# Kernel tuning notes

Hardware: AMD Instinct MI355X
Metric: run time of the kernel (lower is better)

## Reference

```python
import jax, jax.numpy as jnp
import numpy as np

FEAT = 256          # feat_channels == point_feat_channels == in_channels
STACK = 3           # stacked_convs
NPTS = 9            # num_points -> dcn_kernel = 3
NCLS = 80           # num_classes
GM = 0.1            # gradient_mul
GROUPS = 32         # 32 * 256 // 256
EPS = 1e-5
BIAS_CLS = -float(np.log((1 - 0.01) / 0.01))  # prior_prob focal-bias init


def conv2d(x, w, b=None):
    y = jax.lax.conv_general_dilated(x, w, (1, 1), 'SAME',
                                     dimension_numbers=('NCHW', 'OIHW', 'NCHW'))
    return y if b is None else y + b[None, :, None, None]


def group_norm(x, w, b):
    B, C, H, W = x.shape
    xg = x.reshape(B, GROUPS, C // GROUPS, H, W)
    mu = xg.mean((2, 3, 4), keepdims=True)
    var = xg.var((2, 3, 4), keepdims=True)
    xn = ((xg - mu) * jax.lax.rsqrt(var + EPS)).reshape(B, C, H, W)
    return xn * w[None, :, None, None] + b[None, :, None, None]


def bilinear_sample(x, py, px):
    # x: [B,C,H,W]; py,px: [B,K,H,W] absolute sample coords -> [B,C,K,H,W]
    B, C, H, W = x.shape
    y0 = jnp.floor(py); x0 = jnp.floor(px)
    wy = (py - y0)[:, None]; wx = (px - x0)[:, None]  # [B,1,K,H,W]
    xf = x.reshape(B, C, H * W)

    def gather(yi, xi):
        valid = (yi >= 0) & (yi < H) & (xi >= 0) & (xi < W)
        yic = jnp.clip(yi, 0, H - 1).astype(jnp.int32)
        xic = jnp.clip(xi, 0, W - 1).astype(jnp.int32)
        idx = (yic * W + xic).reshape(B, -1)                       # [B,K*H*W]
        g = jax.vmap(lambda xb, ib: xb[:, ib])(xf, idx)            # [B,C,K*H*W]
        g = g.reshape(B, C, *yi.shape[1:])
        return g * valid[:, None].astype(x.dtype)

    v00 = gather(y0, x0); v01 = gather(y0, x0 + 1)
    v10 = gather(y0 + 1, x0); v11 = gather(y0 + 1, x0 + 1)
    return (v00 * (1 - wy) * (1 - wx) + v01 * (1 - wy) * wx
            + v10 * wy * (1 - wx) + v11 * wy * wx)


def deform_conv(x, offset, w):
    # x: [B,C,H,W]; offset: [B,2K,H,W] as (dy,dx) per kernel point; w: [O,C,kh,kw]
    B, C, H, W = x.shape
    O, _, kh, kw = w.shape
    K = kh * kw
    off = offset.reshape(B, K, 2, H, W)
    by = jnp.repeat(jnp.arange(kh) - (kh - 1) // 2, kw).astype(x.dtype)  # [K]
    bx = jnp.tile(jnp.arange(kw) - (kw - 1) // 2, kh).astype(x.dtype)
    gy = jnp.arange(H, dtype=x.dtype)[None, None, :, None]
    gx = jnp.arange(W, dtype=x.dtype)[None, None, None, :]
    py = gy + by[None, :, None, None] + off[:, :, 0]  # [B,K,H,W]
    px = gx + bx[None, :, None, None] + off[:, :, 1]
    sampled = bilinear_sample(x, py, px)              # [B,C,K,H,W]
    return jnp.einsum('bckhw,ock->bohw', sampled, w.reshape(O, C, K))


def dcn_base_offset():
    base = np.arange(-1, 2, dtype=np.float32)
    y = np.repeat(base, 3); x = np.tile(base, 3)
    return jnp.asarray(np.stack([y, x], axis=1).reshape(1, -1, 1, 1))  # [1,18,1,1]


def setup_inputs() -> dict:
    key = jax.random.key(0)
    ks = jax.random.split(key, 10)
    std = 0.01
    d = {}
    d['features'] = jax.random.normal(ks[0], (4, FEAT, 64, 64), jnp.float32)
    d['cls_w'] = std * jax.random.normal(ks[1], (STACK, FEAT, FEAT, 3, 3), jnp.float32)
    d['reg_w'] = std * jax.random.normal(ks[2], (STACK, FEAT, FEAT, 3, 3), jnp.float32)
    d['cls_gn_w'] = jnp.ones((STACK, FEAT), jnp.float32)
    d['cls_gn_b'] = jnp.zeros((STACK, FEAT), jnp.float32)
    d['reg_gn_w'] = jnp.ones((STACK, FEAT), jnp.float32)
    d['reg_gn_b'] = jnp.zeros((STACK, FEAT), jnp.float32)
    d['init_conv_w'] = std * jax.random.normal(ks[3], (FEAT, FEAT, 3, 3), jnp.float32)
    d['init_conv_b'] = jnp.zeros((FEAT,), jnp.float32)
    d['init_out_w'] = std * jax.random.normal(ks[4], (2 * NPTS, FEAT, 1, 1), jnp.float32)
    d['init_out_b'] = jnp.zeros((2 * NPTS,), jnp.float32)
    d['cls_dcn_w'] = std * jax.random.normal(ks[5], (FEAT, FEAT, 3, 3), jnp.float32)
    d['cls_out_w'] = std * jax.random.normal(ks[6], (NCLS, FEAT, 1, 1), jnp.float32)
    d['cls_out_b'] = jnp.full((NCLS,), BIAS_CLS, jnp.float32)
    d['ref_dcn_w'] = std * jax.random.normal(ks[7], (FEAT, FEAT, 3, 3), jnp.float32)
    d['ref_out_w'] = std * jax.random.normal(ks[8], (2 * NPTS, FEAT, 1, 1), jnp.float32)
    d['ref_out_b'] = jnp.zeros((2 * NPTS,), jnp.float32)
    return d


def reference(features, cls_w, reg_w, cls_gn_w, cls_gn_b, reg_gn_w, reg_gn_b,
              init_conv_w, init_conv_b, init_out_w, init_out_b,
              cls_dcn_w, cls_out_w, cls_out_b,
              ref_dcn_w, ref_out_w, ref_out_b):
    cls_feat = reg_feat = features
    for i in range(STACK):
        cls_feat = jax.nn.relu(group_norm(conv2d(cls_feat, cls_w[i]), cls_gn_w[i], cls_gn_b[i]))
        reg_feat = jax.nn.relu(group_norm(conv2d(reg_feat, reg_w[i]), reg_gn_w[i], reg_gn_b[i]))
    pts_init = conv2d(jax.nn.relu(conv2d(reg_feat, init_conv_w, init_conv_b)),
                      init_out_w, init_out_b)                     # [B,18,H,W]
    pts_gm = (1.0 - GM) * jax.lax.stop_gradient(pts_init) + GM * pts_init
    dcn_offset = pts_gm - dcn_base_offset()  # DeformConv adds base back internally
    cls_out = conv2d(jax.nn.relu(deform_conv(cls_feat, dcn_offset, cls_dcn_w)),
                     cls_out_w, cls_out_b)                        # [B,80,H,W]
    pts_refine = conv2d(jax.nn.relu(deform_conv(reg_feat, dcn_offset, ref_dcn_w)),
                        ref_out_w, ref_out_b) + jax.lax.stop_gradient(pts_init)
    # outputs concatenated along channels: [cls(80) | pts_init(18) | pts_refine(18)]
    return jnp.concatenate([cls_out, pts_init, pts_refine], axis=1)
```

## Files before the change

### kernel.cpp

```cpp
#include <hip/hip_runtime.h>

typedef unsigned short u16;
typedef unsigned char u8;
typedef __attribute__((ext_vector_type(8))) short short8;
typedef __attribute__((ext_vector_type(4))) float floatx4;
typedef __attribute__((ext_vector_type(2))) float floatx2;

#define MTOT    16384
#define PADIMG  (66 * 66)
#define PADELEM (4 * PADIMG * 256)
#define PADB    ((size_t)PADELEM * 2)
#define WSTEP   (256 * 2304)

__device__ __forceinline__ float bf2f(u16 u) {
  union { unsigned int i; float f; } c; c.i = ((unsigned int)u) << 16; return c.f;
}
__device__ __forceinline__ u16 f2bf(float f) {
  union { float f; unsigned int i; } c; c.f = f;
  unsigned int r = c.i + 0x7FFFu + ((c.i >> 16) & 1u);
  return (u16)(r >> 16);
}

__device__ __forceinline__ void gl_lds16(const void* g, void* l) {
  __builtin_amdgcn_global_load_lds(
      (const __attribute__((address_space(1))) void*)g,
      (__attribute__((address_space(3))) void*)l, 16, 0, 0);
}

__device__ __forceinline__ int lds_slot32(int row, int q) {
  return row * 32 + ((q ^ ((row >> 1) & 3)) << 3);
}
__device__ __forceinline__ int lds_slot64(int row, int q) {
  return row * 64 + ((q ^ (row & 7)) << 3);
}
__device__ __forceinline__ int lds_slot8(int row, int ks, int quad) {
  return row * 64 + (((ks * 2 + (quad >> 1)) ^ ((row >> 1) & 3)) << 4) + (quad & 1) * 8;
}

__global__ void setup_all(const float* __restrict__ cls_w, const float* __restrict__ reg_w,
                          const float* __restrict__ initw, const float* __restrict__ clsd,
                          const float* __restrict__ refd,
                          const float* __restrict__ iw, const float* __restrict__ cw,
                          const float* __restrict__ rw,
                          const float* __restrict__ features,
                          u16* __restrict__ dst3, u16* __restrict__ dst1,
                          u8* __restrict__ pads8, u8* __restrict__ wf8,
                          u16* __restrict__ padbf) {
  int blk = blockIdx.x;
  int t = threadIdx.x;
  if (blk < 2304) {
    int w = blk >> 8;
    int o = blk & 255;
    const float* src = (w < 3) ? cls_w + (size_t)w * WSTEP
                     : (w < 6) ? reg_w + (size_t)(w - 3) * WSTEP
                     : (w == 6) ? initw : (w == 7) ? clsd : refd;
    __shared__ float wl[2304];
    const float* so = src + (size_t)o * 2304;
    #pragma unroll
    for (int p = 0; p < 9; ++p) wl[p * 256 + t] = so[p * 256 + t];
    __syncthreads();
    if (w == 6) {
      u16* dw = dst3 + (size_t)o * 2304;
      #pragma unroll
      for (int p = 0; p < 9; ++p)
        dw[p * 256 + t] = f2bf(wl[t * 9 + p]);
    } else if (t < 128) {
      int slot = (w < 6) ? w : (w - 1);
      u8* dw8 = wf8 + (size_t)slot * WSTEP + (size_t)o * 2304;
      #pragma unroll
      for (int p = 0; p < 9; ++p) {
        float f0 = wl[(2 * t) * 9 + p] * 64.f;
        float f1 = wl[(2 * t + 1) * 9 + p] * 64.f;
        int pk = __builtin_amdgcn_cvt_pk_fp8_f32(f0, f1, 0, false);
        *(u16*)(dw8 + p * 256 + 2 * t) = (u16)(pk & 0xFFFF);
      }
    }
  } else if (blk < 2688) {
    int bb = blk - 2304;
    int wsel = bb >> 7;
    const float* src = wsel == 0 ? iw : wsel == 1 ? cw : rw;
    int nvalid = wsel == 1 ? 80 : 18;
    float scale = wsel == 0 ? 1.f : (1.f / 64.f);
    int idx = (bb & 127) * 256 + t;
    int o = idx >> 8, c = idx & 255;
    dst1[(size_t)wsel * 32768 + idx] = f2bf(o < nvalid ? src[o * 256 + c] * scale : 0.f);
  } else if (blk < 3712) {
    __shared__ float tile[64][65];
    int bb = blk - 2688;
    int c0 = (bb & 3) * 64;
    int y  = (bb >> 2) & 63;
    int b  = bb >> 8;
    #pragma unroll
    for (int i = 0; i < 16; ++i) {
      int lin = t + i * 256; int c = lin >> 6, x = lin & 63;
      tile[c][x] = features[((b * 256 + c0 + c) * 64 + y) * 64 + x];
    }
    __syncthreads();
    #pragma unroll
    for (int i = 0; i < 8; ++i) {
      int lin = t + i * 256;
      int x = lin >> 5, c2 = lin & 31;
      int pk = __builtin_amdgcn_cvt_pk_fp8_f32(tile[2 * c2][x], tile[2 * c2 + 1][x], 0, false);
      *(u16*)(pads8 + (size_t)((b * 66 + y + 1) * 66 + (x + 1)) * 256 + c0 + 2 * c2) = (u16)pk;
    }
  } else if (blk < 5012) {
    int idx = (blk - 3712) * 256 + t;
    int c4 = (idx & 63) << 2;
    int r = idx >> 6;
    int pix = r % 260;
    int ib = r / 260;
    int y, x;
    if (pix < 66)       { y = 0;  x = pix; }
    else if (pix < 132) { y = 65; x = pix - 66; }
    else if (pix < 196) { y = pix - 132 + 1; x = 0; }
    else                { y = pix - 196 + 1; x = 65; }
    size_t o = (((size_t)ib * PADIMG) + y * 66 + x) * 256 + c4;
    *(unsigned int*)(pads8 + o) = 0u;
  } else {
    int idx = (blk - 5012) * 256 + t;
    int c4 = (idx & 63) << 2;
    int r = idx >> 6;
    int pix = r % 260;
    int b = r / 260;
    int y, x;
    if (pix < 66)       { y = 0;  x = pix; }
    else if (pix < 132) { y = 65; x = pix - 66; }
    else if (pix < 196) { y = pix - 132 + 1; x = 0; }
    else                { y = pix - 196 + 1; x = 65; }
    size_t o = (((size_t)b * PADIMG) + y * 66 + x) * 256 + c4;
    *(ushort4*)(padbf + o) = (ushort4){0, 0, 0, 0};
  }
}

__global__ void __launch_bounds__(256)
gn_apply2(const u16* __restrict__ stage, const float2* __restrict__ st,
          const float* __restrict__ gwc, const float* __restrict__ gbc,
          const float* __restrict__ gwr, const float* __restrict__ gbr,
          u8* __restrict__ cdst8, u8* __restrict__ rdst8, u16* __restrict__ rbf) {
  int tid = blockIdx.x * 256 + threadIdx.x;
  int tower = tid >> 20;
  int r = tid & 0xFFFFF;
  int m = r >> 6, c4 = (r & 63) << 2;
  ushort4 u = *(const ushort4*)(stage + ((size_t)tower << 22) + (size_t)m * 256 + c4);
  int b = m >> 12, p = m & 4095, y = p >> 6, x = p & 63;
  float2 ss = st[tower * 128 + b * 32 + (c4 >> 3)];
  float mu = ss.x * (1.f / 32768.f);
  float var = ss.y * (1.f / 32768.f) - mu * mu;
  float rinv = rsqrtf(var + 1e-5f);
  const float* gw = tower ? gwr : gwc;
  const float* gb = tower ? gbr : gbc;
  float v0 = fmaxf((bf2f(u.x) - mu) * rinv * gw[c4 + 0] + gb[c4 + 0], 0.f);
  float v1 = fmaxf((bf2f(u.y) - mu) * rinv * gw[c4 + 1] + gb[c4 + 1], 0.f);
  float v2 = fmaxf((bf2f(u.z) - mu) * rinv * gw[c4 + 2] + gb[c4 + 2], 0.f);
  float v3 = fmaxf((bf2f(u.w) - mu) * rinv * gw[c4 + 3] + gb[c4 + 3], 0.f);
  size_t pixo = (size_t)((b * 66 + y + 1) * 66 + (x + 1)) * 256 + c4;
  int pk = __builtin_amdgcn_cvt_pk_fp8_f32(v0, v1, 0, false);
  pk = __builtin_amdgcn_cvt_pk_fp8_f32(v2, v3, pk, true);
  *(int*)((tower ? rdst8 : cdst8) + pixo) = pk;
  if (tower && rbf) {
    ushort4 o;
    o.x = f2bf(v0); o.y = f2bf(v1); o.z = f2bf(v2); o.w = f2bf(v3);
    *(ushort4*)(rbf + pixo) = o;
  }
}

__global__ void __launch_bounds__(256)
dcn_sample2(const u8* __restrict__ featC, const u8* __restrict__ featR,
            const float* __restrict__ pts,
            u8* __restrict__ AC, u8* __restrict__ AR) {
  int blk = blockIdx.x;
  const u8* featpad = blk < 1024 ? featC : featR;
  u8* A = blk < 1024 ? AC : AR;
  int mblk = blk & 1023;
  int t = threadIdx.x;
  int m = mblk * 16 + (t >> 4);
  int l = t & 15;
  int b = m >> 12, p = m & 4095, y = p >> 6, x = p & 63;
  const float* pp = pts + (size_t)m * 18;
  const u8* fb = featpad + (size_t)b * PADIMG * 256 + l * 4;
  u8* am = A + (size_t)m * 2304 + l * 4;
  #pragma unroll
  for (int kk = 0; kk < 9; ++kk) {
    float py = (float)y + pp[2 * kk];
    float px = (float)x + pp[2 * kk + 1];
    float fy = floorf(py), fx = floorf(px);
    int y0 = (int)fy, x0 = (int)fx;
    float wy = py - fy, wx = px - fx;
    float w00 = (1.f - wy) * (1.f - wx), w01 = (1.f - wy) * wx;
    float w10 = wy * (1.f - wx), w11 = wy * wx;
    bool yok0 = (unsigned)y0 < 64u, yok1 = (unsigned)(y0 + 1) < 64u;
    bool xok0 = (unsigned)x0 < 64u, xok1 = (unsigned)(x0 + 1) < 64u;
    const u8* base = fb + ((y0 + 1) * 66 + (x0 + 1)) * 256;
    float r[16];
    #pragma unroll
    for (int i = 0; i < 16; ++i) r[i] = 0.f;
    #define ACCUM(OFF, W) { \
      _Pragma("unroll") \
      for (int c = 0; c < 4; ++c) { \
        unsigned int v = *(const unsigned int*)(base + (OFF) + c * 64); \
        floatx2 lo = __builtin_amdgcn_cvt_pk_f32_fp8(v, false); \
        floatx2 hi = __builtin_amdgcn_cvt_pk_f32_fp8(v, true); \
        r[c*4+0] += (W) * lo.x; r[c*4+1] += (W) * lo.y; \
        r[c*4+2] += (W) * hi.x; r[c*4+3] += (W) * hi.y; } }
    if (yok0 & xok0) ACCUM(0, w00)
    if (yok0 & xok1) ACCUM(256, w01)
    if (yok1 & xok0) ACCUM(66 * 256, w10)
    if (yok1 & xok1) ACCUM(67 * 256, w11)
    #undef ACCUM
    #pragma unroll
    for (int c = 0; c < 4; ++c) {
      int pk = __builtin_amdgcn_cvt_pk_fp8_f32(r[c*4+0], r[c*4+1], 0, false);
      pk = __builtin_amdgcn_cvt_pk_fp8_f32(r[c*4+2], r[c*4+3], pk, true);
      *(int*)(am + kk * 256 + c * 64) = pk;
    }
  }
}

template <int AMODE, int EP, int KSZ, int BN, int BK, int NPAIR, int FP8 = 0>
__global__ void __launch_bounds__(256)
gemm_kernel(const u16* __restrict__ A0, const u16* __restrict__ A1,
            const u16* __restrict__ W0, const u16* __restrict__ W1,
            const float* __restrict__ bias0, const float* __restrict__ bias1,
            u16* __restrict__ outb0, u16* __restrict__ outb1,
            float2* __restrict__ st0, float2* __restrict__ st1,
            float* __restrict__ outf,
            const float* __restrict__ addpts0, const float* __restrict__ addpts1,
            float* __restrict__ ptsout0, float* __restrict__ ptsout1,
            int nv0, int nv1, int cb0, int cb1) {
  constexpr int NJ = BN / 32;
  __shared__ u16 As[128 * BK];
  __shared__ u16 Bs[BN * BK];
  int t = threadIdx.x;
  int blk = blockIdx.x;
  int pair = 0;
  if constexpr (NPAIR == 2) { pair = blk & 1; blk >>= 1; }
  const u16* A        = pair ? A1 : A0;
  const u16* Wp       = pair ? W1 : W0;
  const float* bias   = pair ? bias1 : bias0;
  u16* outb           = pair ? outb1 : outb0;
  float2* st          = pair ? st1 : st0;
  const float* addpts = pair ? addpts1 : addpts0;
  float* ptsout       = pair ? ptsout1 : ptsout0;
  int nv = pair ? nv1 : nv0;
  int cb = pair ? cb1 : cb0;

  int bm = blk & 127, bn = blk >> 7;
  int lane = t & 63, wave = t >> 6;
  int wm = (wave & 1) << 6;
  int wn = (wave >> 1) * (BN / 2);
  int quad = lane >> 4, r16 = lane & 15;

  floatx4 acc[4][NJ];
  #pragma unroll
  for (int i = 0; i < 4; ++i)
    #pragma unroll
    for (int j = 0; j < NJ; ++j)
      acc[i][j] = (floatx4){0.f, 0.f, 0.f, 0.f};

  if constexpr (FP8 == 1) {
    u8* As8 = (u8*)As;
    u8* Bs8 = (u8*)Bs;
    const u8* A8 = (const u8*)A;
    const u8* W8 = (const u8*)Wp;
    int row = t >> 2;
    int cq = (t & 3) ^ ((t >> 3) & 3);
    int m0 = bm * 128 + row, m1 = m0 + 64;
    int abase0, abase1;
    if constexpr (AMODE == 1) {
      int b0 = m0 >> 12, p0 = m0 & 4095;
      int b1 = m1 >> 12, p1 = m1 & 4095;
      abase0 = ((b0 * 66 + (p0 >> 6)) * 66 + (p0 & 63)) * 256 + cq * 16;
      abase1 = ((b1 * 66 + (p1 >> 6)) * 66 + (p1 & 63)) * 256 + cq * 16;
    } else {
      abase0 = m0 * KSZ + cq * 16;
      abase1 = m1 * KSZ + cq * 16;
    }
    const u8* wg8 = W8 + (size_t)(bn * BN + row) * KSZ + cq * 16;

    for (int s = 0; s < KSZ / 64; ++s) {
      int d;
      if constexpr (AMODE == 1) {
        int kk = s >> 2;
        int c0 = (s & 3) << 6;
        int ky = kk / 3, kx = kk - ky * 3;
        d = ((ky * 66 + kx) << 8) + c0;
      } else {
        d = s * 64;
      }
      gl_lds16(A8 + abase0 + d, As8 + t * 16);
      gl_lds16(A8 + abase1 + d, As8 + 4096 + t * 16);
      gl_lds16(wg8 + s * 64, Bs8 + t * 16);
      __syncthreads();
      long af8[2][4], bf8[2][NJ];
      #pragma unroll
      for (int ks = 0; ks < 2; ++ks) {
        #pragma unroll
        for (int i = 0; i < 4; ++i)
          af8[ks][i] = *(const long*)&As8[lds_slot8(wm + i * 16 + r16, ks, quad)];
        #pragma unroll
        for (int j = 0; j < NJ; ++j)
          bf8[ks][j] = *(const long*)&Bs8[lds_slot8(wn + j * 16 + r16, ks, quad)];
      }
      #pragma unroll
      for (int ks = 0; ks < 2; ++ks)
        #pragma unroll
        for (int i = 0; i < 4; ++i)
          #pragma unroll
          for (int j = 0; j < NJ; ++j)
            acc[i][j] = __builtin_amdgcn_mfma_f32_16x16x32_fp8_fp8(af8[ks][i], bf8[ks][j], acc[i][j], 0, 0, 0);
      __syncthreads();
    }
  } else if constexpr (BK == 64) {
    int sub = t >> 3;
    int cq = (t & 7) ^ (sub & 7);
    int abase[4];
    #pragma unroll
    for (int k = 0; k < 4; ++k) {
      int m = bm * 128 + k * 32 + sub;
      if constexpr (AMODE == 1) {
        int b = m >> 12, p = m & 4095;
        abase[k] = ((b * 66 + (p >> 6)) * 66 + (p & 63)) * 256 + cq * 8;
      } else {
        abase[k] = m * KSZ + cq * 8;
      }
    }
    const u16* wg = Wp + (size_t)(bn * BN + sub) * KSZ + cq * 8;

    for (int s = 0; s < KSZ / 64; ++s) {
      int d;
      if constexpr (AMODE == 1) {
        int kk = s >> 2;
        int c0 = (s & 3) << 6;
        int ky = kk / 3, kx = kk - ky * 3;
        d = ((ky * 66 + kx) << 8) + c0;
      } else {
        d = s * 64;
      }
      #pragma unroll
      for (int k = 0; k < 4; ++k)
        gl_lds16(A + abase[k] + d, &As[k * 2048 + t * 8]);
      #pragma unroll
      for (int k = 0; k < BN / 32; ++k)
        gl_lds16(wg + (size_t)(k * 32) * KSZ + s * 64, &Bs[k * 2048 + t * 8]);
      __syncthreads();
      short8 af[2][4], bfr[2][NJ];
      #pragma unroll
      for (int ks = 0; ks < 2; ++ks) {
        #pragma unroll
        for (int i = 0; i < 4; ++i)
          af[ks][i] = *(const short8*)&As[lds_slot64(wm + i * 16 + r16, ks * 4 + quad)];
        #pragma unroll
        for (int j = 0; j < NJ; ++j)
          bfr[ks][j] = *(const short8*)&Bs[lds_slot64(wn + j * 16 + r16, ks * 4 + quad)];
      }
      #pragma unroll
      for (int ks = 0; ks < 2; ++ks)
        #pragma unroll
        for (int i = 0; i < 4; ++i)
          #pragma unroll
          for (int j = 0; j < NJ; ++j)
            acc[i][j] = __builtin_amdgcn_mfma_f32_16x16x32_bf16(af[ks][i], bfr[ks][j], acc[i][j], 0, 0, 0);
      __syncthreads();
    }
  } else {
    int row = t >> 2;
    int chunkS = (t & 3) ^ ((t >> 3) & 3);
    int m0 = bm * 128 + row, m1 = m0 + 64;
    int abase0, abase1;
    if constexpr (AMODE == 1) {
      int b0 = m0 >> 12, p0 = m0 & 4095;
      int b1 = m1 >> 12, p1 = m1 & 4095;
      abase0 = ((b0 * 66 + (p0 >> 6)) * 66 + (p0 & 63)) * 256 + chunkS * 8;
      abase1 = ((b1 * 66 + (p1 >> 6)) * 66 + (p1 & 63)) * 256 + chunkS * 8;
    } else {
      abase0 = m0 * KSZ + chunkS * 8;
      abase1 = m1 * KSZ + chunkS * 8;
    }
    const u16* wg = Wp + (size_t)(bn * BN + row) * KSZ + chunkS * 8;

    for (int s = 0; s < KSZ / 32; ++s) {
      int d;
      if constexpr (AMODE == 1) {
        int kk = s >> 3;
        int c0 = (s & 7) << 5;
        int ky = kk / 3, kx = kk - ky * 3;
        d = ((ky * 66 + kx) << 8) + c0;
      } else {
        d = s * 32;
      }
      gl_lds16(A + abase0 + d, &As[t * 8]);
      gl_lds16(A + abase1 + d, &As[2048 + t * 8]);
      gl_lds16(wg + s * 32, &Bs[t * 8]);
      if constexpr (BN == 128)
        gl_lds16(wg + (size_t)64 * KSZ + s * 32, &Bs[2048 + t * 8]);
      __syncthreads();
      short8 af[4], bfr[NJ];
      #pragma unroll
      for (int i = 0; i < 4; ++i)
        af[i] = *(const short8*)&As[lds_slot32(wm + i * 16 + r16, quad)];
      #pragma unroll
      for (int j = 0; j < NJ; ++j)
        bfr[j] = *(const short8*)&Bs[lds_slot32(wn + j * 16 + r16, quad)];
      #pragma unroll
      for (int i = 0; i < 4; ++i)
        #pragma unroll
        for (int j = 0; j < NJ; ++j)
          acc[i][j] = __builtin_amdgcn_mfma_f32_16x16x32_bf16(af[i], bfr[j], acc[i][j], 0, 0, 0);
      __syncthreads();
    }
  }

  #pragma unroll
  for (int j = 0; j < NJ; ++j) {
    int gn = bn * BN + wn + j * 16 + r16;
    float s = 0.f, s2 = 0.f;
    #pragma unroll
    for (int i = 0; i < 4; ++i) {
      #pragma unroll
      for (int r = 0; r < 4; ++r) {
        int gm = bm * 128 + wm + i * 16 + quad * 4 + r;
        float v = acc[i][j][r];
        if constexpr (EP == 0) {
          outb[(size_t)gm * 256 + gn] = f2bf(v);
          s += v; s2 += v * v;
        } else if constexpr (EP == 1) {
          outb[(size_t)gm * 256 + gn] = f2bf(fmaxf(v + bias[gn], 0.f));
        } else if constexpr (EP == 2) {
          outb[(size_t)gm * 256 + gn] = f2bf(fmaxf(v, 0.f));
        } else {
          if (gn < nv) {
            v += bias[gn];
            if (addpts) v += addpts[(size_t)gm * 18 + gn];
            if (ptsout) ptsout[(size_t)gm * 18 + gn] = v;
            int bb = gm >> 12, p = gm & 4095;
            outf[(size_t)((bb * 116 + cb + gn) << 12) + p] = v;
          }
        }
      }
    }
    if constexpr (EP == 0) {
      s += __shfl_xor(s, 1);  s2 += __shfl_xor(s2, 1);
      s += __shfl_xor(s, 2);  s2 += __shfl_xor(s2, 2);
      s += __shfl_xor(s, 4);  s2 += __shfl_xor(s2, 4);
      s += __shfl_xor(s, 16); s2 += __shfl_xor(s2, 16);
      s += __shfl_xor(s, 32); s2 += __shfl_xor(s2, 32);
      if ((lane & 55) == 0) {
        float2* sp = st + ((bm >> 5) * 32) + (gn >> 3);
        atomicAdd(&sp->x, s);
        atomicAdd(&sp->y, s2);
      }
    }
  }
}

extern "C" void kernel_launch(void* const* d_in, const int* in_sizes, int n_in,
                              void* d_out, int out_size, void* d_ws, size_t ws_size,
                              hipStream_t stream) {
  (void)in_sizes; (void)n_in; (void)out_size;
  const float* features    = (const float*)d_in[0];
  const float* cls_w       = (const float*)d_in[1];
  const float* reg_w       = (const float*)d_in[2];
  const float* cls_gn_w    = (const float*)d_in[3];
  const float* cls_gn_b    = (const float*)d_in[4];
  const float* reg_gn_w    = (const float*)d_in[5];
  const float* reg_gn_b    = (const float*)d_in[6];
  const float* init_conv_w = (const float*)d_in[7];
  const float* init_conv_b = (const float*)d_in[8];
  const float* init_out_w  = (const float*)d_in[9];
  const float* init_out_b  = (const float*)d_in[10];
  const float* cls_dcn_w   = (const float*)d_in[11];
  const float* cls_out_w   = (const float*)d_in[12];
  const float* cls_out_b   = (const float*)d_in[13];
  const float* ref_dcn_w   = (const float*)d_in[14];
  const float* ref_out_w   = (const float*)d_in[15];
  const float* ref_out_b   = (const float*)d_in[16];
  float* out = (float*)d_out;

  char* ws = (char*)d_ws;
  size_t off = 0;
  auto alloc = [&](size_t bytes) {
    char* p = ws + off;
    off += (bytes + 255) & ~(size_t)255;
    return p;
  };
  u16* wbf        = (u16*)alloc((size_t)WSTEP * 2);
  u8*  wf8        = (u8*)alloc((size_t)8 * WSTEP);
  u16* w1         = (u16*)alloc((size_t)3 * 32768 * 2);
  u8* xpad8       = (u8*)alloc(PADELEM);
  u8* cpadA8      = (u8*)alloc(PADELEM);
  u8* cpadB8      = (u8*)alloc(PADELEM);
  u8* rpadA8      = (u8*)alloc(PADELEM);
  u8* rpadB8      = (u8*)alloc(PADELEM);
  u16* rpadBF     = (u16*)alloc(PADB);
  float* ptsbuf   = (float*)alloc((size_t)MTOT * 18 * 4);
  float2* statsAll= (float2*)alloc(3 * 256 * sizeof(float2));
  u16* initf      = (u16*)alloc((size_t)MTOT * 256 * 2);
  u16* dcnout     = (u16*)alloc((size_t)2 * MTOT * 256 * 2);
  char* unionReg  = alloc((size_t)MTOT * 2304);
  u16* cstage     = (u16*)unionReg;
  u8* adcn        = (u8*)unionReg;
  u8* adcn2       = (u8*)alloc((size_t)MTOT * 2304);
  bool paired_dcn = (off <= ws_size);

  (void)hipMemsetAsync(statsAll, 0, 3 * 256 * sizeof(float2), stream);
  setup_all<<<5272, 256, 0, stream>>>(cls_w, reg_w, init_conv_w, cls_dcn_w, ref_dcn_w,
                                      init_out_w, cls_out_w, ref_out_w, features,
                                      wbf, w1, xpad8, wf8, rpadBF);

  const u8* curC = xpad8; const u8* curR = xpad8;
  u8* nxtC = cpadA8; u8* altC = cpadB8;
  u8* nxtR = rpadA8; u8* altR = rpadB8;
  for (int i = 0; i < 3; ++i) {
    gemm_kernel<1, 0, 2304, 64, 64, 2, 1><<<1024, 256, 0, stream>>>(
        (const u16*)curC, (const u16*)curR,
        (const u16*)(wf8 + (size_t)i * WSTEP), (const u16*)(wf8 + (size_t)(3 + i) * WSTEP),
        nullptr, nullptr, cstage, cstage + (size_t)MTOT * 256,
        statsAll + i * 256, statsAll + i * 256 + 128,
        nullptr, nullptr, nullptr, nullptr, nullptr, 0, 0, 0, 0);
    gn_apply2<<<8192, 256, 0, stream>>>(cstage, statsAll + i * 256,
        cls_gn_w + i * 256, cls_gn_b + i * 256, reg_gn_w + i * 256, reg_gn_b + i * 256,
        nxtC, nxtR, (i == 2) ? rpadBF : nullptr);
    curC = nxtC; { u8* tmp = nxtC; nxtC = altC; altC = tmp; }
    curR = nxtR; { u8* tmp = nxtR; nxtR = altR; altR = tmp; }
  }
  const u8* cls_feat8 = curC;
  const u8* reg_feat8 = curR;

  gemm_kernel<1, 1, 2304, 32, 64, 1><<<1024, 256, 0, stream>>>(
      rpadBF, nullptr, wbf, nullptr,
      init_conv_b, nullptr, initf, nullptr, nullptr, nullptr,
      nullptr, nullptr, nullptr, nullptr, nullptr, 0, 0, 0, 0);
  gemm_kernel<0, 3, 256, 64, 32, 1><<<256, 256, 0, stream>>>(
      initf, nullptr, w1, nullptr, init_out_b, nullptr,
      nullptr, nullptr, nullptr, nullptr, out,
      nullptr, nullptr, ptsbuf, nullptr, 18, 0, 80, 0);

  if (paired_dcn) {
    dcn_sample2<<<2048, 256, 0, stream>>>(cls_feat8, reg_feat8, ptsbuf, adcn, adcn2);
    gemm_kernel<0, 2, 2304, 64, 64, 2, 1><<<1024, 256, 0, stream>>>(
        (const u16*)adcn, (const u16*)adcn2,
        (const u16*)(wf8 + (size_t)6 * WSTEP), (const u16*)(wf8 + (size_t)7 * WSTEP),
        nullptr, nullptr, dcnout, dcnout + (size_t)MTOT * 256, nullptr, nullptr,
        nullptr, nullptr, nullptr, nullptr, nullptr, 0, 0, 0, 0);
  } else {
    dcn_sample2<<<1024, 256, 0, stream>>>(cls_feat8, cls_feat8, ptsbuf, adcn, adcn);
    gemm_kernel<0, 2, 2304, 64, 64, 1, 1><<<512, 256, 0, stream>>>(
        (const u16*)adcn, nullptr, (const u16*)(wf8 + (size_t)6 * WSTEP), nullptr,
        nullptr, nullptr, dcnout, nullptr, nullptr, nullptr,
        nullptr, nullptr, nullptr, nullptr, nullptr, 0, 0, 0, 0);
    dcn_sample2<<<1024, 256, 0, stream>>>(reg_feat8, reg_feat8, ptsbuf, adcn, adcn);
    gemm_kernel<0, 2, 2304, 64, 64, 1, 1><<<512, 256, 0, stream>>>(
        (const u16*)adcn, nullptr, (const u16*)(wf8 + (size_t)7 * WSTEP), nullptr,
        nullptr, nullptr, dcnout + (size_t)MTOT * 256, nullptr, nullptr, nullptr,
        nullptr, nullptr, nullptr, nullptr, nullptr, 0, 0, 0, 0);
  }

  gemm_kernel<0, 3, 256, 64, 32, 2><<<512, 256, 0, stream>>>(
      dcnout, dcnout + (size_t)MTOT * 256, w1 + 32768, w1 + 2 * 32768,
      cls_out_b, ref_out_b, nullptr, nullptr, nullptr, nullptr, out,
      nullptr, ptsbuf, nullptr, nullptr, 80, 18, 0, 98);
}
```

Measured before the change: 392.8 us.

## Permute fp8 channel layout so MFMA fragments load with 128-bit LDS reads

Reorders fp8 channels within each 64-channel block (weights, padded input features, and GN outputs) so each lane's two k-step fragments sit next to each other. The fp8 GEMM inner loop then issues one 16-byte LDS read per fragment row instead of two 8-byte reads, which halves the LDS read instruction count. The permutation must stay consistent across every producer of fp8 data. Any fp8 producer not updated here, such as the deformable sampler, would silently compute wrong results.

```diff
diff --git a/kernel.cpp b/kernel.cpp
--- a/kernel.cpp
+++ b/kernel.cpp
@@ -5,6 +5,7 @@
 typedef __attribute__((ext_vector_type(8))) short short8;
 typedef __attribute__((ext_vector_type(4))) float floatx4;
 typedef __attribute__((ext_vector_type(2))) float floatx2;
+typedef __attribute__((ext_vector_type(2))) long longx2;
 
 #define MTOT    16384
 #define PADIMG  (66 * 66)
@@ -33,8 +34,11 @@
 __device__ __forceinline__ int lds_slot64(int row, int q) {
   return row * 64 + ((q ^ (row & 7)) << 3);
 }
-__device__ __forceinline__ int lds_slot8(int row, int ks, int quad) {
-  return row * 64 + (((ks * 2 + (quad >> 1)) ^ ((row >> 1) & 3)) << 4) + (quad & 1) * 8;
+__device__ __forceinline__ int lds_slot8r(int row, int quad) {
+  return row * 64 + ((quad ^ ((row >> 1) & 3)) << 4);
+}
+__device__ __forceinline__ int permw(int w) {
+  return ((w >> 3) & 3) * 16 + ((w >> 5) & 1) * 8 + (w & 7);
 }
 
 __global__ void setup_all(const float* __restrict__ cls_w, const float* __restrict__ reg_w,
@@ -67,12 +71,14 @@
     } else if (t < 128) {
       int slot = (w < 6) ? w : (w - 1);
       u8* dw8 = wf8 + (size_t)slot * WSTEP + (size_t)o * 2304;
+      int c = 2 * t;
+      int pos = (c & 192) + permw(c & 63);
       #pragma unroll
       for (int p = 0; p < 9; ++p) {
-        float f0 = wl[(2 * t) * 9 + p] * 64.f;
-        float f1 = wl[(2 * t + 1) * 9 + p] * 64.f;
+        float f0 = wl[c * 9 + p] * 64.f;
+        float f1 = wl[(c + 1) * 9 + p] * 64.f;
         int pk = __builtin_amdgcn_cvt_pk_fp8_f32(f0, f1, 0, false);
-        *(u16*)(dw8 + p * 256 + 2 * t) = (u16)(pk & 0xFFFF);
+        *(u16*)(dw8 + p * 256 + pos) = (u16)(pk & 0xFFFF);
       }
     }
   } else if (blk < 2688) {
@@ -101,7 +107,8 @@
       int lin = t + i * 256;
       int x = lin >> 5, c2 = lin & 31;
       int pk = __builtin_amdgcn_cvt_pk_fp8_f32(tile[2 * c2][x], tile[2 * c2 + 1][x], 0, false);
-      *(u16*)(pads8 + (size_t)((b * 66 + y + 1) * 66 + (x + 1)) * 256 + c0 + 2 * c2) = (u16)pk;
+      *(u16*)(pads8 + (size_t)((b * 66 + y + 1) * 66 + (x + 1)) * 256
+              + c0 + permw(2 * c2)) = (u16)pk;
     }
   } else if (blk < 5012) {
     int idx = (blk - 3712) * 256 + t;
@@ -153,14 +160,14 @@
   float v1 = fmaxf((bf2f(u.y) - mu) * rinv * gw[c4 + 1] + gb[c4 + 1], 0.f);
   float v2 = fmaxf((bf2f(u.z) - mu) * rinv * gw[c4 + 2] + gb[c4 + 2], 0.f);
   float v3 = fmaxf((bf2f(u.w) - mu) * rinv * gw[c4 + 3] + gb[c4 + 3], 0.f);
-  size_t pixo = (size_t)((b * 66 + y + 1) * 66 + (x + 1)) * 256 + c4;
+  size_t pixbase = (size_t)((b * 66 + y + 1) * 66 + (x + 1)) * 256;
   int pk = __builtin_amdgcn_cvt_pk_fp8_f32(v0, v1, 0, false);
   pk = __builtin_amdgcn_cvt_pk_fp8_f32(v2, v3, pk, true);
-  *(int*)((tower ? rdst8 : cdst8) + pixo) = pk;
+  *(int*)((tower ? rdst8 : cdst8) + pixbase + (c4 & 192) + permw(c4 & 63)) = pk;
   if (tower && rbf) {
     ushort4 o;
     o.x = f2bf(v0); o.y = f2bf(v1); o.z = f2bf(v2); o.w = f2bf(v3);
-    *(ushort4*)(rbf + pixo) = o;
+    *(ushort4*)(rbf + pixbase + c4) = o;
   }
 }
 
@@ -228,8 +235,8 @@
             float* __restrict__ ptsout0, float* __restrict__ ptsout1,
             int nv0, int nv1, int cb0, int cb1) {
   constexpr int NJ = BN / 32;
-  __shared__ u16 As[128 * BK];
-  __shared__ u16 Bs[BN * BK];
+  __shared__ __align__(16) u16 As[128 * BK];
+  __shared__ __align__(16) u16 Bs[BN * BK];
   int t = threadIdx.x;
   int blk = blockIdx.x;
   int pair = 0;
@@ -293,13 +300,14 @@
       __syncthreads();
       long af8[2][4], bf8[2][NJ];
       #pragma unroll
-      for (int ks = 0; ks < 2; ++ks) {
-        #pragma unroll
-        for (int i = 0; i < 4; ++i)
-          af8[ks][i] = *(const long*)&As8[lds_slot8(wm + i * 16 + r16, ks, quad)];
-        #pragma unroll
-        for (int j = 0; j < NJ; ++j)
-          bf8[ks][j] = *(const long*)&Bs8[lds_slot8(wn + j * 16 + r16, ks, quad)];
+      for (int i = 0; i < 4; ++i) {
+        longx2 v = *(const longx2*)&As8[lds_slot8r(wm + i * 16 + r16, quad)];
+        af8[0][i] = v.x; af8[1][i] = v.y;
+      }
+      #pragma unroll
+      for (int j = 0; j < NJ; ++j) {
+        longx2 v = *(const longx2*)&Bs8[lds_slot8r(wn + j * 16 + r16, quad)];
+        bf8[0][j] = v.x; bf8[1][j] = v.y;
       }
       #pragma unroll
       for (int ks = 0; ks < 2; ++ks)
```

After: 378.1 us. 1.04x faster.
